# Kernel optimization log

Hardware: AMD Instinct MI355X
Metric: run time of the kernel (lower is better)

The kernel has to match this reference:

```python
import jax, jax.numpy as jnp
import numpy as np

B, S, D, H = 2, 1536, 1024, 16
DK = D // H
NEG = -1e9
WEIGHT = 1.0  # undefined global `Weight` in source; treated as scalar 1.0


def setup_inputs() -> dict:
    key = jax.random.key(0)
    ks = jax.random.split(key, 16)
    inp = {
        "query": jax.random.normal(ks[0], (B, S, D), jnp.float32),
        "key": jax.random.normal(ks[1], (B, S, D), jnp.float32),
        "value": jax.random.normal(ks[2], (B, S, D), jnp.float32),
        "mask": jax.random.randint(ks[3], (B, 1, 1, S), 0, 2, jnp.int32),
        "mask1": jax.random.randint(ks[4], (B, 1, S, S), 0, 2, jnp.int32).astype(jnp.float32),
        "Wq": jax.random.normal(ks[5], (D, D), jnp.float32) / np.sqrt(D),
        "bq": jnp.zeros((D,), jnp.float32),
        "Wk": jax.random.normal(ks[6], (D, D), jnp.float32) / np.sqrt(D),
        "bk": jnp.zeros((D,), jnp.float32),
        "Wv": jax.random.normal(ks[7], (D, D), jnp.float32) / np.sqrt(D),
        "bv": jnp.zeros((D,), jnp.float32),
        "Wo": jax.random.normal(ks[8], (D, D), jnp.float32) / np.sqrt(D),
        "bo": jnp.zeros((D,), jnp.float32),
    }
    return inp


def _split_heads(x):
    # [B,S,D] -> [B,H,S,DK]
    return x.reshape(B, S, H, DK).transpose(0, 2, 1, 3)


def reference(query, key, value, mask, mask1, Wq, bq, Wk, bk, Wv, bv, Wo, bo):
    q = _split_heads(query @ Wq.T + bq)
    k = _split_heads(key @ Wk.T + bk)
    v = _split_heads(value @ Wv.T + bv)

    scores = jnp.einsum("bhqd,bhkd->bhqk", q, k) / jnp.sqrt(jnp.float32(DK))
    # softmax of mask1 over the query axis (dim=-2), zeros masked out
    m1 = jnp.where(mask1 == 0, NEG, mask1)
    m1s = jax.nn.softmax(m1, axis=-2)
    scores = (1.0 + m1s * mask1) * scores * WEIGHT
    scores = jnp.where(mask == 0, NEG, scores)
    p = jax.nn.softmax(scores, axis=-1)  # dropout: eval mode (identity)
    x = jnp.einsum("bhqk,bhkd->bhqd", p, v)
    x = x.transpose(0, 2, 1, 3).reshape(B, S, D)
    ret = x @ Wo.T + bo
    return ret, scores
```

## Files before the change

kernel.cpp:

```cpp
#include <hip/hip_runtime.h>
#include <hip/hip_bf16.h>

#define B_ 2
#define S_ 1536
#define D_ 1024
#define H_ 16
#define DK_ 64
#define KW_ 48
#define NT_ 24

#define RET_ELEMS 3145728

typedef __attribute__((ext_vector_type(8))) short short8;
typedef __attribute__((ext_vector_type(8))) unsigned short ushort8v;
typedef __attribute__((ext_vector_type(4))) unsigned short ushort4v;
typedef __attribute__((ext_vector_type(4))) float f32x4;

__device__ __forceinline__ unsigned short bf16_rne(float f) {
    return __builtin_bit_cast(unsigned short, __float2bfloat16(f));
}

struct CvtJobs {
    const float* src[7];
    unsigned short* dst[7];
    int n8[7];
};

__global__ __launch_bounds__(256) void cvt_kernel(CvtJobs j) {
    const int y = blockIdx.y;
    const int i = blockIdx.x * 256 + threadIdx.x;
    if (i >= j.n8[y]) return;
    const float* s = j.src[y] + (size_t)i * 8;
    float4 f0 = *(const float4*)s;
    float4 f1 = *(const float4*)(s + 4);
    ushort8v u;
    u[0]=bf16_rne(f0.x); u[1]=bf16_rne(f0.y); u[2]=bf16_rne(f0.z); u[3]=bf16_rne(f0.w);
    u[4]=bf16_rne(f1.x); u[5]=bf16_rne(f1.y); u[6]=bf16_rne(f1.z); u[7]=bf16_rne(f1.w);
    *(ushort8v*)(j.dst[y] + (size_t)i * 8) = u;
}

__global__ void bitpack_kernel(const float* __restrict__ mask1, unsigned int* __restrict__ bits) {
    const size_t gid = (size_t)blockIdx.x * 256 + threadIdx.x;
    const float v = mask1[gid];
    const unsigned long long bal = __ballot(v != 0.f);
    const int l = threadIdx.x & 63;
    if (l == 0)       bits[gid >> 5] = (unsigned int)bal;
    else if (l == 32) bits[gid >> 5] = (unsigned int)(bal >> 32);
}

__global__ void colcount_bits_kernel(const unsigned int* __restrict__ bits, float* __restrict__ colsum) {
    const int b   = blockIdx.x >> 3;
    const int col = ((blockIdx.x & 7) * 256 + threadIdx.x) & (S_ - 1);
    const int wword = col >> 5, bit = col & 31;
    const unsigned int* p = bits + (size_t)b * S_ * KW_ + wword;
    int s = 0;
    for (int q = 0; q < S_; ++q) s += (p[(size_t)q * KW_] >> bit) & 1u;
    colsum[b * S_ + col] = (float)s;
}

struct Proj { const unsigned short* A; const unsigned short* W; const float* bias; unsigned short* C; };

__global__ __launch_bounds__(512) void qkv_gemm_kernel(Proj p0, Proj p1, Proj p2) {
    const int z = blockIdx.z;
    const unsigned short* A = z == 0 ? p0.A    : (z == 1 ? p1.A    : p2.A);
    const unsigned short* W = z == 0 ? p0.W    : (z == 1 ? p1.W    : p2.W);
    const float* bias       = z == 0 ? p0.bias : (z == 1 ? p1.bias : p2.bias);
    unsigned short* C       = z == 0 ? p0.C    : (z == 1 ? p1.C    : p2.C);

    __shared__ unsigned short As[128][72];
    __shared__ unsigned short Bs[128][72];
    const int tid = threadIdx.x;
    const int w = tid >> 6, lane = tid & 63;
    const int g = lane >> 4, c = lane & 15;
    const int wm = w >> 2, wn = w & 3;
    const int m0 = blockIdx.y * 128, n0 = blockIdx.x * 128;
    const int trow = tid >> 2;
    const int tcol = (tid & 3) * 16;

    f32x4 acc[4][2];
    #pragma unroll
    for (int m = 0; m < 4; ++m)
        #pragma unroll
        for (int n = 0; n < 2; ++n)
            acc[m][n] = f32x4{0.f, 0.f, 0.f, 0.f};

    for (int k0 = 0; k0 < D_; k0 += 64) {
        {
            const unsigned short* ap = A + (size_t)(m0 + trow) * D_ + k0 + tcol;
            *(ushort8v*)&As[trow][tcol]     = *(const ushort8v*)ap;
            *(ushort8v*)&As[trow][tcol + 8] = *(const ushort8v*)(ap + 8);
            const unsigned short* wp = W + (size_t)(n0 + trow) * D_ + k0 + tcol;
            *(ushort8v*)&Bs[trow][tcol]     = *(const ushort8v*)wp;
            *(ushort8v*)&Bs[trow][tcol + 8] = *(const ushort8v*)(wp + 8);
        }
        __syncthreads();
        #pragma unroll
        for (int kk = 0; kk < 2; ++kk) {
            short8 a[4], bb[2];
            #pragma unroll
            for (int m = 0; m < 4; ++m) a[m]  = *(const short8*)&As[wm * 64 + m * 16 + c][kk * 32 + g * 8];
            #pragma unroll
            for (int n = 0; n < 2; ++n) bb[n] = *(const short8*)&Bs[wn * 32 + n * 16 + c][kk * 32 + g * 8];
            #pragma unroll
            for (int m = 0; m < 4; ++m)
                #pragma unroll
                for (int n = 0; n < 2; ++n)
                    acc[m][n] = __builtin_amdgcn_mfma_f32_16x16x32_bf16(a[m], bb[n], acc[m][n], 0, 0, 0);
        }
        __syncthreads();
    }
    #pragma unroll
    for (int n = 0; n < 2; ++n) {
        const int col = n0 + wn * 32 + n * 16 + c;
        const float bval = bias[col];
        #pragma unroll
        for (int m = 0; m < 4; ++m) {
            const int row0 = m0 + wm * 64 + m * 16 + g * 4;
            #pragma unroll
            for (int r = 0; r < 4; ++r)
                C[(size_t)(row0 + r) * D_ + col] = bf16_rne(acc[m][n][r] + bval);
        }
    }
}

__global__ __launch_bounds__(256) void out_gemm_kernel(
    const unsigned short* __restrict__ A, const unsigned short* __restrict__ W,
    const float* __restrict__ bias, float* __restrict__ C)
{
    __shared__ unsigned short As[64][72];
    __shared__ unsigned short Bs[64][72];
    const int tid = threadIdx.x;
    const int w = tid >> 6, lane = tid & 63;
    const int g = lane >> 4, c = lane & 15;
    const int wm = w >> 1, wn = w & 1;
    const int m0 = blockIdx.y * 64, n0 = blockIdx.x * 64;
    const int trow = tid >> 2;
    const int tcol = (tid & 3) * 16;

    f32x4 acc[2][2];
    #pragma unroll
    for (int m = 0; m < 2; ++m)
        #pragma unroll
        for (int n = 0; n < 2; ++n)
            acc[m][n] = f32x4{0.f, 0.f, 0.f, 0.f};

    for (int k0 = 0; k0 < D_; k0 += 64) {
        {
            const unsigned short* ap = A + (size_t)(m0 + trow) * D_ + k0 + tcol;
            *(ushort8v*)&As[trow][tcol]     = *(const ushort8v*)ap;
            *(ushort8v*)&As[trow][tcol + 8] = *(const ushort8v*)(ap + 8);
            const unsigned short* wp = W + (size_t)(n0 + trow) * D_ + k0 + tcol;
            *(ushort8v*)&Bs[trow][tcol]     = *(const ushort8v*)wp;
            *(ushort8v*)&Bs[trow][tcol + 8] = *(const ushort8v*)(wp + 8);
        }
        __syncthreads();
        #pragma unroll
        for (int kk = 0; kk < 2; ++kk) {
            short8 a[2], bb[2];
            #pragma unroll
            for (int m = 0; m < 2; ++m) a[m]  = *(const short8*)&As[wm * 32 + m * 16 + c][kk * 32 + g * 8];
            #pragma unroll
            for (int n = 0; n < 2; ++n) bb[n] = *(const short8*)&Bs[wn * 32 + n * 16 + c][kk * 32 + g * 8];
            #pragma unroll
            for (int m = 0; m < 2; ++m)
                #pragma unroll
                for (int n = 0; n < 2; ++n)
                    acc[m][n] = __builtin_amdgcn_mfma_f32_16x16x32_bf16(a[m], bb[n], acc[m][n], 0, 0, 0);
        }
        __syncthreads();
    }
    #pragma unroll
    for (int n = 0; n < 2; ++n) {
        const int col = n0 + wn * 32 + n * 16 + c;
        const float bval = bias[col];
        #pragma unroll
        for (int m = 0; m < 2; ++m) {
            const int row0 = m0 + wm * 32 + m * 16 + g * 4;
            #pragma unroll
            for (int r = 0; r < 4; ++r)
                C[(size_t)(row0 + r) * D_ + col] = acc[m][n][r] + bval;
        }
    }
}

__global__ __launch_bounds__(256) void attn_kernel(
    const unsigned short* __restrict__ Qb, const unsigned short* __restrict__ Kb,
    const unsigned short* __restrict__ Vb, const int* __restrict__ mask,
    const unsigned int* __restrict__ bits, const float* __restrict__ colsum,
    float* __restrict__ scores, unsigned short* __restrict__ X)
{
    const int qt = blockIdx.x;
    const int h  = blockIdx.y;
    const int b  = blockIdx.z;
    const int tid = threadIdx.x;
    const int w = tid >> 6, lane = tid & 63;
    const int g = lane >> 4, c = lane & 15;

    __shared__ unsigned short VT_lds[2][64][72];
    __shared__ unsigned short P_lds[4][16][72];
    __shared__ float fac_lds[S_];

    for (int i = tid; i < S_; i += 256) {
        const int km = mask[b * S_ + i];
        const float cnt = colsum[b * S_ + i];
        fac_lds[i] = (km == 0) ? -1.f : ((cnt > 0.f) ? (1.f / cnt) : 0.f);
    }

    const int qrow0 = qt * 64 + w * 16;
    const unsigned short* qptr = Qb + ((size_t)b * S_ + qrow0 + c) * D_ + h * DK_;
    const short8 qf0 = *(const short8*)(qptr + g * 8);
    const short8 qf1 = *(const short8*)(qptr + 32 + g * 8);

    float mrow = -INFINITY, lrow = 0.f;
    f32x4 o[4];
    #pragma unroll
    for (int n = 0; n < 4; ++n) o[n] = f32x4{0.f, 0.f, 0.f, 0.f};

    float* srow = scores + ((((size_t)(b * H_ + h)) * S_ + qrow0 + c) * S_);
    const unsigned int* brow = bits + ((size_t)b * S_ + qrow0 + c) * KW_;
    const int kr = tid & 63, half = tid >> 6;
    const unsigned short* vrow = Vb + ((size_t)b * S_ + kr) * D_ + h * DK_ + half * 16;

    {
        short8 v0 = *(const short8*)vrow;
        short8 v1 = *(const short8*)(vrow + 8);
        #pragma unroll
        for (int j = 0; j < 8; ++j) {
            VT_lds[0][half * 16 + j][kr]     = (unsigned short)v0[j];
            VT_lds[0][half * 16 + 8 + j][kr] = (unsigned short)v1[j];
        }
    }
    __syncthreads();

    for (int kt = 0; kt < NT_; ++kt) {
        const int k0 = kt * 64;
        const int cur = kt & 1;
        const bool have_next = (kt + 1) < NT_;

        short8 nv0, nv1;
        if (have_next) {
            const unsigned short* vs = vrow + (size_t)(k0 + 64) * D_;
            nv0 = *(const short8*)vs;
            nv1 = *(const short8*)(vs + 8);
        }

        f32x4 sacc[4];
        #pragma unroll
        for (int n = 0; n < 4; ++n) sacc[n] = f32x4{0.f, 0.f, 0.f, 0.f};
        #pragma unroll
        for (int n = 0; n < 4; ++n) {
            const unsigned short* kp = Kb + ((size_t)b * S_ + k0 + n * 16 + c) * D_ + h * DK_;
            short8 kf0 = *(const short8*)(kp + g * 8);
            short8 kf1 = *(const short8*)(kp + 32 + g * 8);
            sacc[n] = __builtin_amdgcn_mfma_f32_16x16x32_bf16(kf0, qf0, sacc[n], 0, 0, 0);
            sacc[n] = __builtin_amdgcn_mfma_f32_16x16x32_bf16(kf1, qf1, sacc[n], 0, 0, 0);
        }

        const unsigned int w0 = brow[(k0 >> 5)];
        const unsigned int w1 = brow[(k0 >> 5) + 1];
        float pmax = -INFINITY;
        f32x4 sv[4];
        #pragma unroll
        for (int n = 0; n < 4; ++n) {
            const f32x4 fv = *(const f32x4*)&fac_lds[k0 + n * 16 + g * 4];
            const unsigned int wsel = (n < 2) ? w0 : w1;
            #pragma unroll
            for (int r = 0; r < 4; ++r) {
                const int kl = n * 16 + g * 4 + r;
                const float f = fv[r];
                const float icnt = fmaxf(f, 0.f);
                const float bit = (float)((wsel >> (kl & 31)) & 1u);
                float s = sacc[n][r] * 0.125f * (1.f + bit * icnt);
                s = (f < 0.f) ? -1e9f : s;
                sv[n][r] = s;
                pmax = fmaxf(pmax, s);
            }
            __builtin_nontemporal_store(sv[n], (f32x4*)&srow[k0 + n * 16 + g * 4]);
        }

        pmax = fmaxf(pmax, __shfl_xor(pmax, 16));
        pmax = fmaxf(pmax, __shfl_xor(pmax, 32));
        const float nm = fmaxf(mrow, pmax);
        const float scq = __expf(mrow - nm);
        mrow = nm;
        lrow *= scq;
        float sc_o[4];
        #pragma unroll
        for (int r = 0; r < 4; ++r) sc_o[r] = __shfl(scq, (lane & 48) | (g * 4 + r));
        #pragma unroll
        for (int n = 0; n < 4; ++n)
            #pragma unroll
            for (int r = 0; r < 4; ++r) o[n][r] *= sc_o[r];

        #pragma unroll
        for (int n = 0; n < 4; ++n) {
            ushort4v pu;
            #pragma unroll
            for (int r = 0; r < 4; ++r) {
                const float p = __expf(sv[n][r] - mrow);
                lrow += p;
                pu[r] = bf16_rne(p);
            }
            *(ushort4v*)&P_lds[w][c][n * 16 + g * 4] = pu;
        }

        if (have_next) {
            #pragma unroll
            for (int j = 0; j < 8; ++j) {
                VT_lds[cur ^ 1][half * 16 + j][kr]     = (unsigned short)nv0[j];
                VT_lds[cur ^ 1][half * 16 + 8 + j][kr] = (unsigned short)nv1[j];
            }
        }

        #pragma unroll
        for (int kk = 0; kk < 2; ++kk) {
            const short8 pa = *(const short8*)&P_lds[w][c][kk * 32 + g * 8];
            #pragma unroll
            for (int n = 0; n < 4; ++n) {
                const short8 vf = *(const short8*)&VT_lds[cur][n * 16 + c][kk * 32 + g * 8];
                o[n] = __builtin_amdgcn_mfma_f32_16x16x32_bf16(pa, vf, o[n], 0, 0, 0);
            }
        }
        __syncthreads();
    }

    lrow += __shfl_xor(lrow, 16);
    lrow += __shfl_xor(lrow, 32);
    const float linv = 1.f / lrow;
    float linv_o[4];
    #pragma unroll
    for (int r = 0; r < 4; ++r) linv_o[r] = __shfl(linv, (lane & 48) | (g * 4 + r));
    #pragma unroll
    for (int n = 0; n < 4; ++n)
        #pragma unroll
        for (int r = 0; r < 4; ++r) {
            const size_t idx = ((size_t)b * S_ + qrow0 + g * 4 + r) * D_ + h * DK_ + n * 16 + c;
            X[idx] = bf16_rne(o[n][r] * linv_o[r]);
        }
}

extern "C" void kernel_launch(void* const* d_in, const int* in_sizes, int n_in,
                              void* d_out, int out_size, void* d_ws, size_t ws_size,
                              hipStream_t stream) {
    const float* query = (const float*)d_in[0];
    const float* key   = (const float*)d_in[1];
    const float* value = (const float*)d_in[2];
    const int*   mask  = (const int*)d_in[3];
    const float* mask1 = (const float*)d_in[4];
    const float* Wq = (const float*)d_in[5];
    const float* bq = (const float*)d_in[6];
    const float* Wk = (const float*)d_in[7];
    const float* bk = (const float*)d_in[8];
    const float* Wv = (const float*)d_in[9];
    const float* bv = (const float*)d_in[10];
    const float* Wo = (const float*)d_in[11];
    const float* bo = (const float*)d_in[12];

    float* ret_out    = (float*)d_out;
    float* scores_out = ret_out + RET_ELEMS;

    const size_t SZ = (size_t)B_ * S_ * D_;
    const size_t WZ = (size_t)D_ * D_;
    float* colsum = (float*)d_ws;
    unsigned int* bits = (unsigned int*)((char*)d_ws + 16384);
    unsigned short* Qb  = (unsigned short*)((char*)d_ws + 16384 + 589824);
    unsigned short* Kb  = Qb + SZ;
    unsigned short* Vb  = Kb + SZ;
    unsigned short* Xb  = Vb + SZ;
    unsigned short* qf  = Xb + SZ;
    unsigned short* kf  = qf + SZ;
    unsigned short* vf  = kf + SZ;
    unsigned short* Wqb = vf + SZ;
    unsigned short* Wkb = Wqb + WZ;
    unsigned short* Wvb = Wkb + WZ;
    unsigned short* Wob = Wvb + WZ;

    CvtJobs jobs;
    jobs.src[0] = query; jobs.dst[0] = qf;  jobs.n8[0] = (int)(SZ / 8);
    jobs.src[1] = key;   jobs.dst[1] = kf;  jobs.n8[1] = (int)(SZ / 8);
    jobs.src[2] = value; jobs.dst[2] = vf;  jobs.n8[2] = (int)(SZ / 8);
    jobs.src[3] = Wq;    jobs.dst[3] = Wqb; jobs.n8[3] = (int)(WZ / 8);
    jobs.src[4] = Wk;    jobs.dst[4] = Wkb; jobs.n8[4] = (int)(WZ / 8);
    jobs.src[5] = Wv;    jobs.dst[5] = Wvb; jobs.n8[5] = (int)(WZ / 8);
    jobs.src[6] = Wo;    jobs.dst[6] = Wob; jobs.n8[6] = (int)(WZ / 8);
    cvt_kernel<<<dim3((int)(SZ / 8 / 256), 7), 256, 0, stream>>>(jobs);

    bitpack_kernel<<<(B_ * S_ * S_) / 256, 256, 0, stream>>>(mask1, bits);
    colcount_bits_kernel<<<16, 256, 0, stream>>>(bits, colsum);

    Proj p0{qf, Wqb, bq, Qb}, p1{kf, Wkb, bk, Kb}, p2{vf, Wvb, bv, Vb};
    qkv_gemm_kernel<<<dim3(D_ / 128, (B_ * S_) / 128, 3), 512, 0, stream>>>(p0, p1, p2);

    attn_kernel<<<dim3(S_ / 64, H_, B_), 256, 0, stream>>>(Qb, Kb, Vb, mask, bits, colsum, scores_out, Xb);

    out_gemm_kernel<<<dim3(D_ / 64, (B_ * S_) / 64), 256, 0, stream>>>(Xb, Wob, bo, ret_out);
}
```

Before: 235.0 us.

## Remap grids per XCD, split column counting, enlarge attention tiles, add MFMA priority

Several changes land together. The column-count kernel is split across 16 row chunks and combined with atomic adds, with colsum zeroed inside bitpack, which gives it far more parallelism than 16 blocks. The GEMM and attention launches become 1D grids, remapped so neighbouring tiles land on the same XCD for better L2 reuse. The attention block grows to 512 threads with 128 query rows, so each K/V tile is shared by more warps. s_setprio is raised around MFMA sections. Risks include float atomics, lower occupancy from the larger blocks, and the hard-coded block mappings.

```diff
diff --git a/kernel.cpp b/kernel.cpp
--- a/kernel.cpp
+++ b/kernel.cpp
@@ -39,7 +39,9 @@
     *(ushort8v*)(j.dst[y] + (size_t)i * 8) = u;
 }
 
-__global__ void bitpack_kernel(const float* __restrict__ mask1, unsigned int* __restrict__ bits) {
+__global__ void bitpack_kernel(const float* __restrict__ mask1, unsigned int* __restrict__ bits,
+                               float* __restrict__ colsum) {
+    if (blockIdx.x < 12) colsum[blockIdx.x * 256 + threadIdx.x] = 0.f;
     const size_t gid = (size_t)blockIdx.x * 256 + threadIdx.x;
     const float v = mask1[gid];
     const unsigned long long bal = __ballot(v != 0.f);
@@ -49,19 +51,27 @@
 }
 
 __global__ void colcount_bits_kernel(const unsigned int* __restrict__ bits, float* __restrict__ colsum) {
-    const int b   = blockIdx.x >> 3;
-    const int col = ((blockIdx.x & 7) * 256 + threadIdx.x) & (S_ - 1);
+    const int b     = blockIdx.x / 6;
+    const int chunk = blockIdx.x % 6;
+    const int col   = chunk * 256 + threadIdx.x;
+    const int q0    = blockIdx.y * 96;
     const int wword = col >> 5, bit = col & 31;
-    const unsigned int* p = bits + (size_t)b * S_ * KW_ + wword;
+    const unsigned int* p = bits + ((size_t)b * S_ + q0) * KW_ + wword;
     int s = 0;
-    for (int q = 0; q < S_; ++q) s += (p[(size_t)q * KW_] >> bit) & 1u;
-    colsum[b * S_ + col] = (float)s;
+    #pragma unroll 8
+    for (int q = 0; q < 96; ++q) s += (p[(size_t)q * KW_] >> bit) & 1u;
+    atomicAdd(&colsum[b * S_ + col], (float)s);
 }
 
 struct Proj { const unsigned short* A; const unsigned short* W; const float* bias; unsigned short* C; };
 
 __global__ __launch_bounds__(512) void qkv_gemm_kernel(Proj p0, Proj p1, Proj p2) {
-    const int z = blockIdx.z;
+    const int bid = blockIdx.x;
+    const int xcd = bid & 7, idx = bid >> 3;
+    const int zy = xcd * 9 + (idx >> 3);
+    const int bx = idx & 7;
+    const int z = zy / 24, by = zy % 24;
+
     const unsigned short* A = z == 0 ? p0.A    : (z == 1 ? p1.A    : p2.A);
     const unsigned short* W = z == 0 ? p0.W    : (z == 1 ? p1.W    : p2.W);
     const float* bias       = z == 0 ? p0.bias : (z == 1 ? p1.bias : p2.bias);
@@ -73,7 +83,7 @@
     const int w = tid >> 6, lane = tid & 63;
     const int g = lane >> 4, c = lane & 15;
     const int wm = w >> 2, wn = w & 3;
-    const int m0 = blockIdx.y * 128, n0 = blockIdx.x * 128;
+    const int m0 = by * 128, n0 = bx * 128;
     const int trow = tid >> 2;
     const int tcol = (tid & 3) * 16;
 
@@ -101,11 +111,13 @@
             for (int m = 0; m < 4; ++m) a[m]  = *(const short8*)&As[wm * 64 + m * 16 + c][kk * 32 + g * 8];
             #pragma unroll
             for (int n = 0; n < 2; ++n) bb[n] = *(const short8*)&Bs[wn * 32 + n * 16 + c][kk * 32 + g * 8];
+            __builtin_amdgcn_s_setprio(1);
             #pragma unroll
             for (int m = 0; m < 4; ++m)
                 #pragma unroll
                 for (int n = 0; n < 2; ++n)
                     acc[m][n] = __builtin_amdgcn_mfma_f32_16x16x32_bf16(a[m], bb[n], acc[m][n], 0, 0, 0);
+            __builtin_amdgcn_s_setprio(0);
         }
         __syncthreads();
     }
@@ -127,13 +139,18 @@
     const unsigned short* __restrict__ A, const unsigned short* __restrict__ W,
     const float* __restrict__ bias, float* __restrict__ C)
 {
+    const int bid = blockIdx.x;
+    const int xcd = bid & 7, idx = bid >> 3;
+    const int yg = xcd * 6 + (idx >> 4);
+    const int bx = idx & 15;
+
     __shared__ unsigned short As[64][72];
     __shared__ unsigned short Bs[64][72];
     const int tid = threadIdx.x;
     const int w = tid >> 6, lane = tid & 63;
     const int g = lane >> 4, c = lane & 15;
     const int wm = w >> 1, wn = w & 1;
-    const int m0 = blockIdx.y * 64, n0 = blockIdx.x * 64;
+    const int m0 = yg * 64, n0 = bx * 64;
     const int trow = tid >> 2;
     const int tcol = (tid & 3) * 16;
 
@@ -161,11 +178,13 @@
             for (int m = 0; m < 2; ++m) a[m]  = *(const short8*)&As[wm * 32 + m * 16 + c][kk * 32 + g * 8];
             #pragma unroll
             for (int n = 0; n < 2; ++n) bb[n] = *(const short8*)&Bs[wn * 32 + n * 16 + c][kk * 32 + g * 8];
+            __builtin_amdgcn_s_setprio(1);
             #pragma unroll
             for (int m = 0; m < 2; ++m)
                 #pragma unroll
                 for (int n = 0; n < 2; ++n)
                     acc[m][n] = __builtin_amdgcn_mfma_f32_16x16x32_bf16(a[m], bb[n], acc[m][n], 0, 0, 0);
+            __builtin_amdgcn_s_setprio(0);
         }
         __syncthreads();
     }
@@ -183,30 +202,33 @@
     }
 }
 
-__global__ __launch_bounds__(256) void attn_kernel(
+__global__ __launch_bounds__(512) void attn_kernel(
     const unsigned short* __restrict__ Qb, const unsigned short* __restrict__ Kb,
     const unsigned short* __restrict__ Vb, const int* __restrict__ mask,
     const unsigned int* __restrict__ bits, const float* __restrict__ colsum,
     float* __restrict__ scores, unsigned short* __restrict__ X)
 {
-    const int qt = blockIdx.x;
-    const int h  = blockIdx.y;
-    const int b  = blockIdx.z;
+    const int bid = blockIdx.x;
+    const int xcd = bid & 7, idx = bid >> 3;
+    const int grp = xcd * 4 + idx / 12;
+    const int qt  = idx % 12;
+    const int h = grp & 15, b = grp >> 4;
+
     const int tid = threadIdx.x;
     const int w = tid >> 6, lane = tid & 63;
     const int g = lane >> 4, c = lane & 15;
 
     __shared__ unsigned short VT_lds[2][64][72];
-    __shared__ unsigned short P_lds[4][16][72];
+    __shared__ unsigned short P_lds[8][16][72];
     __shared__ float fac_lds[S_];
 
-    for (int i = tid; i < S_; i += 256) {
+    for (int i = tid; i < S_; i += 512) {
         const int km = mask[b * S_ + i];
         const float cnt = colsum[b * S_ + i];
         fac_lds[i] = (km == 0) ? -1.f : ((cnt > 0.f) ? (1.f / cnt) : 0.f);
     }
 
-    const int qrow0 = qt * 64 + w * 16;
+    const int qrow0 = qt * 128 + w * 16;
     const unsigned short* qptr = Qb + ((size_t)b * S_ + qrow0 + c) * D_ + h * DK_;
     const short8 qf0 = *(const short8*)(qptr + g * 8);
     const short8 qf1 = *(const short8*)(qptr + 32 + g * 8);
@@ -219,16 +241,13 @@
     float* srow = scores + ((((size_t)(b * H_ + h)) * S_ + qrow0 + c) * S_);
     const unsigned int* brow = bits + ((size_t)b * S_ + qrow0 + c) * KW_;
     const int kr = tid & 63, half = tid >> 6;
-    const unsigned short* vrow = Vb + ((size_t)b * S_ + kr) * D_ + h * DK_ + half * 16;
+    const unsigned short* vrow = Vb + ((size_t)b * S_ + kr) * D_ + h * DK_ + half * 8;
 
     {
         short8 v0 = *(const short8*)vrow;
-        short8 v1 = *(const short8*)(vrow + 8);
-        #pragma unroll
-        for (int j = 0; j < 8; ++j) {
-            VT_lds[0][half * 16 + j][kr]     = (unsigned short)v0[j];
-            VT_lds[0][half * 16 + 8 + j][kr] = (unsigned short)v1[j];
-        }
+        #pragma unroll
+        for (int j = 0; j < 8; ++j)
+            VT_lds[0][half * 8 + j][kr] = (unsigned short)v0[j];
     }
     __syncthreads();
 
@@ -237,24 +256,26 @@
         const int cur = kt & 1;
         const bool have_next = (kt + 1) < NT_;
 
-        short8 nv0, nv1;
-        if (have_next) {
-            const unsigned short* vs = vrow + (size_t)(k0 + 64) * D_;
-            nv0 = *(const short8*)vs;
-            nv1 = *(const short8*)(vs + 8);
-        }
+        short8 nv0;
+        if (have_next) nv0 = *(const short8*)(vrow + (size_t)(k0 + 64) * D_);
 
         f32x4 sacc[4];
         #pragma unroll
         for (int n = 0; n < 4; ++n) sacc[n] = f32x4{0.f, 0.f, 0.f, 0.f};
+        short8 kf0[4], kf1[4];
         #pragma unroll
         for (int n = 0; n < 4; ++n) {
             const unsigned short* kp = Kb + ((size_t)b * S_ + k0 + n * 16 + c) * D_ + h * DK_;
-            short8 kf0 = *(const short8*)(kp + g * 8);
-            short8 kf1 = *(const short8*)(kp + 32 + g * 8);
-            sacc[n] = __builtin_amdgcn_mfma_f32_16x16x32_bf16(kf0, qf0, sacc[n], 0, 0, 0);
-            sacc[n] = __builtin_amdgcn_mfma_f32_16x16x32_bf16(kf1, qf1, sacc[n], 0, 0, 0);
-        }
+            kf0[n] = *(const short8*)(kp + g * 8);
+            kf1[n] = *(const short8*)(kp + 32 + g * 8);
+        }
+        __builtin_amdgcn_s_setprio(1);
+        #pragma unroll
+        for (int n = 0; n < 4; ++n) {
+            sacc[n] = __builtin_amdgcn_mfma_f32_16x16x32_bf16(kf0[n], qf0, sacc[n], 0, 0, 0);
+            sacc[n] = __builtin_amdgcn_mfma_f32_16x16x32_bf16(kf1[n], qf1, sacc[n], 0, 0, 0);
+        }
+        __builtin_amdgcn_s_setprio(0);
 
         const unsigned int w0 = brow[(k0 >> 5)];
         const unsigned int w1 = brow[(k0 >> 5) + 1];
@@ -306,12 +327,11 @@
 
         if (have_next) {
             #pragma unroll
-            for (int j = 0; j < 8; ++j) {
-                VT_lds[cur ^ 1][half * 16 + j][kr]     = (unsigned short)nv0[j];
-                VT_lds[cur ^ 1][half * 16 + 8 + j][kr] = (unsigned short)nv1[j];
-            }
-        }
-
+            for (int j = 0; j < 8; ++j)
+                VT_lds[cur ^ 1][half * 8 + j][kr] = (unsigned short)nv0[j];
+        }
+
+        __builtin_amdgcn_s_setprio(1);
         #pragma unroll
         for (int kk = 0; kk < 2; ++kk) {
             const short8 pa = *(const short8*)&P_lds[w][c][kk * 32 + g * 8];
@@ -321,6 +341,7 @@
                 o[n] = __builtin_amdgcn_mfma_f32_16x16x32_bf16(pa, vf, o[n], 0, 0, 0);
             }
         }
+        __builtin_amdgcn_s_setprio(0);
         __syncthreads();
     }
 
@@ -385,13 +406,13 @@
     jobs.src[6] = Wo;    jobs.dst[6] = Wob; jobs.n8[6] = (int)(WZ / 8);
     cvt_kernel<<<dim3((int)(SZ / 8 / 256), 7), 256, 0, stream>>>(jobs);
 
-    bitpack_kernel<<<(B_ * S_ * S_) / 256, 256, 0, stream>>>(mask1, bits);
-    colcount_bits_kernel<<<16, 256, 0, stream>>>(bits, colsum);
+    bitpack_kernel<<<(B_ * S_ * S_) / 256, 256, 0, stream>>>(mask1, bits, colsum);
+    colcount_bits_kernel<<<dim3(12, 16), 256, 0, stream>>>(bits, colsum);
 
     Proj p0{qf, Wqb, bq, Qb}, p1{kf, Wkb, bk, Kb}, p2{vf, Wvb, bv, Vb};
-    qkv_gemm_kernel<<<dim3(D_ / 128, (B_ * S_) / 128, 3), 512, 0, stream>>>(p0, p1, p2);
-
-    attn_kernel<<<dim3(S_ / 64, H_, B_), 256, 0, stream>>>(Qb, Kb, Vb, mask, bits, colsum, scores_out, Xb);
-
-    out_gemm_kernel<<<dim3(D_ / 64, (B_ * S_) / 64), 256, 0, stream>>>(Xb, Wob, bo, ret_out);
-}
+    qkv_gemm_kernel<<<576, 512, 0, stream>>>(p0, p1, p2);
+
+    attn_kernel<<<384, 512, 0, stream>>>(Qb, Kb, Vb, mask, bits, colsum, scores_out, Xb);
+
+    out_gemm_kernel<<<768, 256, 0, stream>>>(Xb, Wob, bo, ret_out);
+}
```

Measured after the change: 232.3 us. About the same (-1.1%).
